# Kernel optimization log

Hardware: AMD Instinct MI355X
Metric: run time of the kernel (lower is better)

The kernel has to match this reference:

```python
import jax, jax.numpy as jnp
import numpy as np

NUM_HEADS = 12
WIN = 7  # window_size[0] == window_size[1]


def setup_inputs() -> dict:
    key = jax.random.key(0)
    ks = jax.random.split(key, 8)
    B_, N, C = 2048, WIN * WIN, 384
    nW = 64
    return {
        "x": jax.random.normal(ks[0], (B_, N, C), dtype=jnp.float32),
        "mask": jax.random.normal(ks[1], (nW, N, N), dtype=jnp.float32),
        "qkv_w": jax.random.normal(ks[2], (3 * C, C), dtype=jnp.float32) * 0.02,
        "qkv_b": jax.random.normal(ks[3], (3 * C,), dtype=jnp.float32) * 0.02,
        "proj_w": jax.random.normal(ks[4], (C, C), dtype=jnp.float32) * 0.02,
        "proj_b": jax.random.normal(ks[5], (C,), dtype=jnp.float32) * 0.02,
        "rpb_table": jax.random.normal(ks[6], ((2 * WIN - 1) ** 2, NUM_HEADS), dtype=jnp.float32) * 0.02,
        "rel_index": jax.random.randint(ks[7], (N * N,), 0, (2 * WIN - 1) ** 2, dtype=jnp.int32),
    }


def reference(x, mask, qkv_w, qkv_b, proj_w, proj_b, rpb_table, rel_index):
    B_, N, C = x.shape
    H = NUM_HEADS
    d = C // H
    scale = d ** -0.5

    # QKV projection (quant wrappers act as identity in non-quant state)
    qkv = x @ qkv_w.T + qkv_b                      # [B_, N, 3C]
    qkv = qkv.reshape(B_, N, 3, H, d).transpose(2, 0, 3, 1, 4)  # [3, B_, H, N, d]
    q, k, v = qkv[0], qkv[1], qkv[2]

    attn = jnp.einsum("bhnd,bhmd->bhnm", q * scale, k)  # [B_, H, N, N]

    # relative position bias gather: [N*N] -> [N, N, H] -> [H, N, N]
    bias = rpb_table[rel_index].reshape(N, N, H).transpose(2, 0, 1)
    attn = attn + bias[None]

    # shifted-window mask add
    nW = mask.shape[0]
    attn = attn.reshape(B_ // nW, nW, H, N, N) + mask[None, :, None]
    attn = attn.reshape(B_, H, N, N)

    attn = jax.nn.softmax(attn, axis=-1)

    out = jnp.einsum("bhnm,bhmd->bhnd", attn, v)   # [B_, H, N, d]
    out = out.transpose(0, 2, 1, 3).reshape(B_, N, C)
    out = out @ proj_w.T + proj_b
    return out, attn
```

## Files before the change

kernel.cpp:

```cpp
#include <hip/hip_runtime.h>
#include <hip/hip_bf16.h>
#include <stdint.h>

#define H_ 12
#define D_ 32
#define N_ 49
#define C_ 384
#define B_TOT 2048
#define BH 24576
#define M_ROWS 100352
#define SCALE 0.17677669529663689f

typedef float f32x4 __attribute__((ext_vector_type(4)));
typedef __bf16 bf16x8 __attribute__((ext_vector_type(8)));
typedef unsigned short ushortx8 __attribute__((ext_vector_type(8)));

static __device__ __forceinline__ unsigned short f2bf(float f) {
  __bf16 b = (__bf16)f;
  return __builtin_bit_cast(unsigned short, b);
}

static __device__ __forceinline__ uint4 pack8(float4 a, float4 b) {
  ushortx8 v;
  v[0] = f2bf(a.x); v[1] = f2bf(a.y); v[2] = f2bf(a.z); v[3] = f2bf(a.w);
  v[4] = f2bf(b.x); v[5] = f2bf(b.y); v[6] = f2bf(b.z); v[7] = f2bf(b.w);
  return __builtin_bit_cast(uint4, v);
}

#define GL16(gp, lp)                                                        \
  __builtin_amdgcn_global_load_lds(                                         \
      (const __attribute__((address_space(1))) unsigned int*)(gp),          \
      (__attribute__((address_space(3))) unsigned int*)(lp), 16, 0, 0)

__global__ void prep(const float* __restrict__ x, const float* __restrict__ wq,
                     const float* __restrict__ wpw, const float* __restrict__ mask,
                     const float* __restrict__ rpb, const int* __restrict__ ridx,
                     unsigned short* __restrict__ x_bf,
                     unsigned short* __restrict__ wq_bf,
                     unsigned short* __restrict__ wp_bf,
                     float* __restrict__ comb) {
  const int blk = blockIdx.x, tid = threadIdx.x;
  if (blk < 2048) {
    for (int i = blk * 256 + tid; i < 4816896; i += 2048 * 256) {
      float4 a = ((const float4*)x)[2 * i];
      float4 b = ((const float4*)x)[2 * i + 1];
      *(uint4*)&x_bf[(size_t)i * 8] = pack8(a, b);
    }
  } else if (blk < 2264) {
    const int i = (blk - 2048) * 256 + tid;
    float4 a = ((const float4*)wq)[2 * i];
    float4 b = ((const float4*)wq)[2 * i + 1];
    *(uint4*)&wq_bf[(size_t)i * 8] = pack8(a, b);
  } else if (blk < 2336) {
    const int i = (blk - 2264) * 256 + tid;
    float4 a = ((const float4*)wpw)[2 * i];
    float4 b = ((const float4*)wpw)[2 * i + 1];
    *(uint4*)&wp_bf[(size_t)i * 8] = pack8(a, b);
  } else {
    const int wh = blk - 2336;
    const int w = wh / 12, h = wh - w * 12;
    float* cb = comb + (size_t)wh * 4096;
    const float* mw = mask + (size_t)w * N_ * N_;
    for (int e = tid; e < 4096; e += 256) {
      const int r = e >> 6, c = e & 63;
      float v;
      if (c >= N_) v = -1e30f;
      else if (r >= N_) v = 0.0f;
      else v = mw[r * N_ + c] + rpb[ridx[r * N_ + c] * H_ + h];
      cb[(r * 16 + (c & 15)) * 4 + (c >> 4)] = v;
    }
  }
}

__global__ __launch_bounds__(256, 4)
void qkv_gemm(const unsigned short* __restrict__ A,
              const unsigned short* __restrict__ W,
              const float* __restrict__ bias, unsigned short* __restrict__ qkv) {
  __shared__ __align__(16) unsigned short smem[16384];
  const int tid = threadIdx.x;
  const int w = blockIdx.x;
  const int t = (w & 7) * 882 + (w >> 3);
  const int bm = t / 9, bn = t - bm * 9;
  const int lane = tid & 63, wv = tid >> 6;
  const int wm = wv >> 1, wn = wv & 1;
  const int lo = lane & 15, hi = lane >> 4;

  const int sr0 = tid >> 2, sq0 = (tid & 3) ^ ((sr0 >> 1) & 3);
  const int ci1 = tid + 256;
  const int sr1 = ci1 >> 2, sq1 = (ci1 & 3) ^ ((sr1 >> 1) & 3);

  const unsigned short* Ab = A + (size_t)bm * 128 * 384;
  const unsigned short* Wb = W + (size_t)bn * 128 * 384;

  f32x4 acc[4][4];
#pragma unroll
  for (int i = 0; i < 4; i++)
#pragma unroll
    for (int j = 0; j < 4; j++)
#pragma unroll
      for (int r = 0; r < 4; r++) acc[i][j][r] = 0.0f;

  {
    unsigned short* b0 = smem;
    GL16(Ab + sr0 * 384 + sq0 * 8, b0 + tid * 8);
    GL16(Ab + sr1 * 384 + sq1 * 8, b0 + ci1 * 8);
    GL16(Wb + sr0 * 384 + sq0 * 8, b0 + 4096 + tid * 8);
    GL16(Wb + sr1 * 384 + sq1 * 8, b0 + 4096 + ci1 * 8);
  }
  __syncthreads();

  int buf = 0;
  for (int kt = 0; kt < 12; kt++) {
    if (kt < 11) {
      const int kk = (kt + 1) * 32;
      unsigned short* nb = smem + (buf ^ 1) * 8192;
      GL16(Ab + sr0 * 384 + kk + sq0 * 8, nb + tid * 8);
      GL16(Ab + sr1 * 384 + kk + sq1 * 8, nb + ci1 * 8);
      GL16(Wb + sr0 * 384 + kk + sq0 * 8, nb + 4096 + tid * 8);
      GL16(Wb + sr1 * 384 + kk + sq1 * 8, nb + 4096 + ci1 * 8);
    }
    const unsigned short* ba = smem + buf * 8192;
    bf16x8 af[4], bfm[4];
#pragma unroll
    for (int mt = 0; mt < 4; mt++) {
      const int row = wm * 64 + mt * 16 + lo;
      af[mt] = *(const bf16x8*)&ba[(row * 4 + (hi ^ ((row >> 1) & 3))) * 8];
    }
#pragma unroll
    for (int nt = 0; nt < 4; nt++) {
      const int row = wn * 64 + nt * 16 + lo;
      bfm[nt] = *(const bf16x8*)&ba[4096 + (row * 4 + (hi ^ ((row >> 1) & 3))) * 8];
    }
#pragma unroll
    for (int mt = 0; mt < 4; mt++)
#pragma unroll
      for (int nt = 0; nt < 4; nt++)
        acc[mt][nt] = __builtin_amdgcn_mfma_f32_16x16x32_bf16(af[mt], bfm[nt], acc[mt][nt], 0, 0, 0);
    __syncthreads();
    buf ^= 1;
  }

  unsigned short* ep = smem + wv * 4096;
#pragma unroll
  for (int nt = 0; nt < 4; nt++) {
    const int j = bn * 128 + wn * 64 + nt * 16 + lo;
    const float bj = bias[j];
    const float mul = (j < 384) ? SCALE : 1.0f;
    const int c16 = nt * 2 + (lo >> 3);
    const int wi = lo & 7;
#pragma unroll
    for (int mt = 0; mt < 4; mt++) {
#pragma unroll
      for (int r = 0; r < 4; r++) {
        const int row = mt * 16 + hi * 4 + r;
        ep[row * 64 + ((c16 ^ hi) << 3) + wi] = f2bf((acc[mt][nt][r] + bj) * mul);
      }
    }
  }
#pragma unroll
  for (int cc = 0; cc < 2; cc++) {
    const int cidx = cc * 64 + lane;
    const int lr = cidx >> 1, lch = cidx & 1;
    const int i = bm * 128 + wm * 64 + lr;
    const int b = i / 49, sq = i - b * 49;
    const int j0 = bn * 128 + wn * 64 + lch * 32;
    const int which = j0 / 384;
    const int rem = j0 - which * 384;
    const int h = rem >> 5;
    const int hlr = (lr >> 2) & 3;
    unsigned short* dst = qkv + ((size_t)which * BH + (size_t)b * H_ + h) * (N_ * D_) + sq * D_;
#pragma unroll
    for (int q = 0; q < 4; q++) {
      const int c16r = lch * 4 + q;
      *(uint4*)(dst + q * 8) = *(const uint4*)&ep[lr * 64 + ((c16r ^ hlr) << 3)];
    }
  }
}

__global__ __launch_bounds__(64, 2)
void attn_kernel(const unsigned short* __restrict__ qkv,
                 const float* __restrict__ comb,
                 float* __restrict__ probs,
                 unsigned short* __restrict__ av) {
  __shared__ __align__(16) unsigned short P[64 * 64];
  __shared__ __align__(16) unsigned short VT[32 * 64];
  const int lane = threadIdx.x;
  const int lo = lane & 15, hi = lane >> 4;
  const int l7 = lo & 7;
  const int h = blockIdx.x, b = blockIdx.y;

  const unsigned short* qp = qkv + (size_t)(b * H_ + h) * (N_ * D_);
  const unsigned short* kp = qp + (size_t)BH * (N_ * D_);
  const unsigned short* vp = kp + (size_t)BH * (N_ * D_);

  {
    unsigned int* vz = (unsigned int*)VT;
#pragma unroll
    for (int i = 0; i < 16; i++) vz[lane + 64 * i] = 0u;
  }
  __syncthreads();

  bf16x8 aq[4], bk[4];
#pragma unroll
  for (int t = 0; t < 4; t++) {
    aq[t] = *(const bf16x8*)(qp + (t * 16 + lo) * D_ + hi * 8);
    bk[t] = *(const bf16x8*)(kp + (t * 16 + lo) * D_ + hi * 8);
  }
  f32x4 s[4][4];
#pragma unroll
  for (int mt = 0; mt < 4; mt++)
#pragma unroll
    for (int nt = 0; nt < 4; nt++) {
#pragma unroll
      for (int r = 0; r < 4; r++) s[mt][nt][r] = 0.0f;
      s[mt][nt] = __builtin_amdgcn_mfma_f32_16x16x32_bf16(aq[mt], bk[nt], s[mt][nt], 0, 0, 0);
    }

#pragma unroll
  for (int it = 0; it < 4; it++) {
    const int idx = it * 64 + lane;
    if (idx < 196) {
      const int sq = idx >> 2, ch = idx & 3;
      ushortx8 vv = *(const ushortx8*)(vp + sq * D_ + ch * 8);
#pragma unroll
      for (int jj = 0; jj < 8; jj++)
        VT[(ch * 8 + jj) * 64 + (((sq >> 3) ^ jj) << 3) + (sq & 7)] = vv[jj];
    }
  }

  const float* cb = comb + (size_t)((b & 63) * H_ + h) * 4096;
#pragma unroll
  for (int mt = 0; mt < 4; mt++) {
#pragma unroll
    for (int r = 0; r < 4; r++) {
      const int row = mt * 16 + hi * 4 + r;
      const float4 cr = *(const float4*)(cb + (row * 16 + lo) * 4);
      float v0 = s[mt][0][r] + cr.x;
      float v1 = s[mt][1][r] + cr.y;
      float v2 = s[mt][2][r] + cr.z;
      float v3 = s[mt][3][r] + cr.w;
      float m = fmaxf(fmaxf(v0, v1), fmaxf(v2, v3));
      m = fmaxf(m, __shfl_xor(m, 1));
      m = fmaxf(m, __shfl_xor(m, 2));
      m = fmaxf(m, __shfl_xor(m, 4));
      m = fmaxf(m, __shfl_xor(m, 8));
      v0 = __expf(v0 - m); v1 = __expf(v1 - m);
      v2 = __expf(v2 - m); v3 = __expf(v3 - m);
      float sum = v0 + v1 + v2 + v3;
      sum += __shfl_xor(sum, 1);
      sum += __shfl_xor(sum, 2);
      sum += __shfl_xor(sum, 4);
      sum += __shfl_xor(sum, 8);
      const float rinv = 1.0f / sum;
      s[mt][0][r] = v0 * rinv; s[mt][1][r] = v1 * rinv;
      s[mt][2][r] = v2 * rinv; s[mt][3][r] = v3 * rinv;
    }
  }

  const size_t pbase = (size_t)(b * H_ + h) * N_ * N_;
#pragma unroll
  for (int mt = 0; mt < 4; mt++) {
#pragma unroll
    for (int r = 0; r < 4; r++) {
      const int row = mt * 16 + hi * 4 + r;
      if (row < N_) {
#pragma unroll
        for (int nt = 0; nt < 4; nt++) {
          const int c = nt * 16 + lo;
          if (c < N_) probs[pbase + row * N_ + c] = s[mt][nt][r];
        }
      }
      const int r7 = row & 7;
#pragma unroll
      for (int nt = 0; nt < 4; nt++)
        P[row * 64 + (((nt * 2 + (lo >> 3)) ^ r7) << 3) + l7] = f2bf(s[mt][nt][r]);
    }
  }
  __syncthreads();

  f32x4 o[4][2];
#pragma unroll
  for (int mt = 0; mt < 4; mt++)
#pragma unroll
    for (int n2 = 0; n2 < 2; n2++)
#pragma unroll
      for (int r = 0; r < 4; r++) o[mt][n2][r] = 0.0f;
#pragma unroll
  for (int ks = 0; ks < 2; ks++) {
    bf16x8 pa[4], vb[2];
#pragma unroll
    for (int mt = 0; mt < 4; mt++)
      pa[mt] = *(const bf16x8*)&P[(mt * 16 + lo) * 64 + (((ks * 4 + hi) ^ l7) << 3)];
#pragma unroll
    for (int n2 = 0; n2 < 2; n2++)
      vb[n2] = *(const bf16x8*)&VT[(n2 * 16 + lo) * 64 + (((ks * 4 + hi) ^ l7) << 3)];
#pragma unroll
    for (int mt = 0; mt < 4; mt++)
#pragma unroll
      for (int n2 = 0; n2 < 2; n2++)
        o[mt][n2] = __builtin_amdgcn_mfma_f32_16x16x32_bf16(pa[mt], vb[n2], o[mt][n2], 0, 0, 0);
  }

  __syncthreads();
#pragma unroll
  for (int mt = 0; mt < 4; mt++) {
#pragma unroll
    for (int r = 0; r < 4; r++) {
      const int row = mt * 16 + hi * 4 + r;
      if (row < N_) {
#pragma unroll
        for (int n2 = 0; n2 < 2; n2++)
          P[row * 40 + n2 * 16 + lo] = f2bf(o[mt][n2][r]);
      }
    }
  }
  if (lane < N_) {
    unsigned short* dst = av + ((size_t)b * N_ + lane) * C_ + h * D_;
    const unsigned short* src = P + lane * 40;
#pragma unroll
    for (int q = 0; q < 4; q++)
      *(uint4*)(dst + q * 8) = *(const uint4*)(src + q * 8);
  }
}

__global__ __launch_bounds__(256, 4)
void proj_gemm(const unsigned short* __restrict__ A,
               const unsigned short* __restrict__ W,
               const float* __restrict__ bias, float* __restrict__ out) {
  __shared__ __align__(16) unsigned short smem[16384];
  const int tid = threadIdx.x;
  const int w = blockIdx.x;
  const int t = (w & 7) * 294 + (w >> 3);
  const int bm = t / 3, bn = t - bm * 3;
  const int lane = tid & 63, wv = tid >> 6;
  const int wm = wv >> 1, wn = wv & 1;
  const int lo = lane & 15, hi = lane >> 4;

  const int sr0 = tid >> 2, sq0 = (tid & 3) ^ ((sr0 >> 1) & 3);
  const int ci1 = tid + 256;
  const int sr1 = ci1 >> 2, sq1 = (ci1 & 3) ^ ((sr1 >> 1) & 3);

  const unsigned short* Ab = A + (size_t)bm * 128 * 384;
  const unsigned short* Wb = W + (size_t)bn * 128 * 384;

  f32x4 acc[4][4];
#pragma unroll
  for (int i = 0; i < 4; i++)
#pragma unroll
    for (int j = 0; j < 4; j++)
#pragma unroll
      for (int r = 0; r < 4; r++) acc[i][j][r] = 0.0f;

  {
    unsigned short* b0 = smem;
    GL16(Ab + sr0 * 384 + sq0 * 8, b0 + tid * 8);
    GL16(Ab + sr1 * 384 + sq1 * 8, b0 + ci1 * 8);
    GL16(Wb + sr0 * 384 + sq0 * 8, b0 + 4096 + tid * 8);
    GL16(Wb + sr1 * 384 + sq1 * 8, b0 + 4096 + ci1 * 8);
  }
  __syncthreads();

  int buf = 0;
  for (int kt = 0; kt < 12; kt++) {
    if (kt < 11) {
      const int kk = (kt + 1) * 32;
      unsigned short* nb = smem + (buf ^ 1) * 8192;
      GL16(Ab + sr0 * 384 + kk + sq0 * 8, nb + tid * 8);
      GL16(Ab + sr1 * 384 + kk + sq1 * 8, nb + ci1 * 8);
      GL16(Wb + sr0 * 384 + kk + sq0 * 8, nb + 4096 + tid * 8);
      GL16(Wb + sr1 * 384 + kk + sq1 * 8, nb + 4096 + ci1 * 8);
    }
    const unsigned short* ba = smem + buf * 8192;
    bf16x8 af[4], bfm[4];
#pragma unroll
    for (int mt = 0; mt < 4; mt++) {
      const int row = wm * 64 + mt * 16 + lo;
      af[mt] = *(const bf16x8*)&ba[(row * 4 + (hi ^ ((row >> 1) & 3))) * 8];
    }
#pragma unroll
    for (int nt = 0; nt < 4; nt++) {
      const int row = wn * 64 + nt * 16 + lo;
      bfm[nt] = *(const bf16x8*)&ba[4096 + (row * 4 + (hi ^ ((row >> 1) & 3))) * 8];
    }
#pragma unroll
    for (int mt = 0; mt < 4; mt++)
#pragma unroll
      for (int nt = 0; nt < 4; nt++)
        acc[mt][nt] = __builtin_amdgcn_mfma_f32_16x16x32_bf16(af[mt], bfm[nt], acc[mt][nt], 0, 0, 0);
    __syncthreads();
    buf ^= 1;
  }

#pragma unroll
  for (int nt = 0; nt < 4; nt++) {
    const int j = bn * 128 + wn * 64 + nt * 16 + lo;
    const float bj = bias[j];
#pragma unroll
    for (int mt = 0; mt < 4; mt++) {
#pragma unroll
      for (int r = 0; r < 4; r++) {
        const int i = bm * 128 + wm * 64 + mt * 16 + hi * 4 + r;
        out[(size_t)i * 384 + j] = acc[mt][nt][r] + bj;
      }
    }
  }
}

extern "C" void kernel_launch(void* const* d_in, const int* in_sizes, int n_in,
                              void* d_out, int out_size, void* d_ws, size_t ws_size,
                              hipStream_t stream) {
  const float* x      = (const float*)d_in[0];
  const float* mask   = (const float*)d_in[1];
  const float* qkv_w  = (const float*)d_in[2];
  const float* qkv_b  = (const float*)d_in[3];
  const float* proj_w = (const float*)d_in[4];
  const float* proj_b = (const float*)d_in[5];
  const float* rpb    = (const float*)d_in[6];
  const int*   ridx   = (const int*)d_in[7];

  unsigned short* qkv   = (unsigned short*)d_ws;
  unsigned short* x_bf  = qkv + (size_t)3 * BH * N_ * D_;
  unsigned short* av    = x_bf;
  float* comb           = (float*)(x_bf + (size_t)M_ROWS * C_);
  unsigned short* wq_bf = (unsigned short*)(comb + 768 * 4096);
  unsigned short* wp_bf = wq_bf + 1152 * 384;
  float* out   = (float*)d_out;
  float* probs = out + (size_t)M_ROWS * C_;

  prep<<<3104, 256, 0, stream>>>(x, qkv_w, proj_w, mask, rpb, ridx,
                                 x_bf, wq_bf, wp_bf, comb);
  qkv_gemm<<<7056, 256, 0, stream>>>(x_bf, wq_bf, qkv_b, qkv);
  attn_kernel<<<dim3(H_, B_TOT), 64, 0, stream>>>(qkv, comb, probs, av);
  proj_gemm<<<2352, 256, 0, stream>>>(av, wp_bf, proj_b, out);
}
```

Before: 458.4 us.

## Split attention kernel across four waves, one 16-row query tile each

```diff
diff --git a/kernel.cpp b/kernel.cpp
--- a/kernel.cpp
+++ b/kernel.cpp
@@ -177,14 +177,15 @@
   }
 }
 
-__global__ __launch_bounds__(64, 2)
+__global__ __launch_bounds__(256, 8)
 void attn_kernel(const unsigned short* __restrict__ qkv,
                  const float* __restrict__ comb,
                  float* __restrict__ probs,
                  unsigned short* __restrict__ av) {
   __shared__ __align__(16) unsigned short P[64 * 64];
   __shared__ __align__(16) unsigned short VT[32 * 64];
-  const int lane = threadIdx.x;
+  const int tid = threadIdx.x;
+  const int wv = tid >> 6, lane = tid & 63;
   const int lo = lane & 15, hi = lane >> 4;
   const int l7 = lo & 7;
   const int h = blockIdx.x, b = blockIdx.y;
@@ -196,127 +197,100 @@
   {
     unsigned int* vz = (unsigned int*)VT;
 #pragma unroll
-    for (int i = 0; i < 16; i++) vz[lane + 64 * i] = 0u;
-  }
-  __syncthreads();
-
-  bf16x8 aq[4], bk[4];
-#pragma unroll
-  for (int t = 0; t < 4; t++) {
-    aq[t] = *(const bf16x8*)(qp + (t * 16 + lo) * D_ + hi * 8);
+    for (int i = 0; i < 8; i++) vz[tid + 256 * i] = 0u;
+  }
+  __syncthreads();
+
+  bf16x8 aq = *(const bf16x8*)(qp + (wv * 16 + lo) * D_ + hi * 8);
+  bf16x8 bk[4];
+#pragma unroll
+  for (int t = 0; t < 4; t++)
     bk[t] = *(const bf16x8*)(kp + (t * 16 + lo) * D_ + hi * 8);
-  }
-  f32x4 s[4][4];
-#pragma unroll
-  for (int mt = 0; mt < 4; mt++)
-#pragma unroll
-    for (int nt = 0; nt < 4; nt++) {
-#pragma unroll
-      for (int r = 0; r < 4; r++) s[mt][nt][r] = 0.0f;
-      s[mt][nt] = __builtin_amdgcn_mfma_f32_16x16x32_bf16(aq[mt], bk[nt], s[mt][nt], 0, 0, 0);
-    }
-
-#pragma unroll
-  for (int it = 0; it < 4; it++) {
-    const int idx = it * 64 + lane;
-    if (idx < 196) {
-      const int sq = idx >> 2, ch = idx & 3;
-      ushortx8 vv = *(const ushortx8*)(vp + sq * D_ + ch * 8);
-#pragma unroll
-      for (int jj = 0; jj < 8; jj++)
-        VT[(ch * 8 + jj) * 64 + (((sq >> 3) ^ jj) << 3) + (sq & 7)] = vv[jj];
-    }
+
+  f32x4 s[4];
+#pragma unroll
+  for (int nt = 0; nt < 4; nt++) {
+#pragma unroll
+    for (int r = 0; r < 4; r++) s[nt][r] = 0.0f;
+    s[nt] = __builtin_amdgcn_mfma_f32_16x16x32_bf16(aq, bk[nt], s[nt], 0, 0, 0);
+  }
+
+  if (tid < 196) {
+    const int sq = tid >> 2, ch = tid & 3;
+    ushortx8 vv = *(const ushortx8*)(vp + sq * D_ + ch * 8);
+#pragma unroll
+    for (int jj = 0; jj < 8; jj++)
+      VT[(ch * 8 + jj) * 64 + (((sq >> 3) ^ jj) << 3) + (sq & 7)] = vv[jj];
   }
 
   const float* cb = comb + (size_t)((b & 63) * H_ + h) * 4096;
-#pragma unroll
-  for (int mt = 0; mt < 4; mt++) {
-#pragma unroll
-    for (int r = 0; r < 4; r++) {
-      const int row = mt * 16 + hi * 4 + r;
-      const float4 cr = *(const float4*)(cb + (row * 16 + lo) * 4);
-      float v0 = s[mt][0][r] + cr.x;
-      float v1 = s[mt][1][r] + cr.y;
-      float v2 = s[mt][2][r] + cr.z;
-      float v3 = s[mt][3][r] + cr.w;
-      float m = fmaxf(fmaxf(v0, v1), fmaxf(v2, v3));
-      m = fmaxf(m, __shfl_xor(m, 1));
-      m = fmaxf(m, __shfl_xor(m, 2));
-      m = fmaxf(m, __shfl_xor(m, 4));
-      m = fmaxf(m, __shfl_xor(m, 8));
-      v0 = __expf(v0 - m); v1 = __expf(v1 - m);
-      v2 = __expf(v2 - m); v3 = __expf(v3 - m);
-      float sum = v0 + v1 + v2 + v3;
-      sum += __shfl_xor(sum, 1);
-      sum += __shfl_xor(sum, 2);
-      sum += __shfl_xor(sum, 4);
-      sum += __shfl_xor(sum, 8);
-      const float rinv = 1.0f / sum;
-      s[mt][0][r] = v0 * rinv; s[mt][1][r] = v1 * rinv;
-      s[mt][2][r] = v2 * rinv; s[mt][3][r] = v3 * rinv;
-    }
-  }
-
   const size_t pbase = (size_t)(b * H_ + h) * N_ * N_;
 #pragma unroll
-  for (int mt = 0; mt < 4; mt++) {
-#pragma unroll
-    for (int r = 0; r < 4; r++) {
-      const int row = mt * 16 + hi * 4 + r;
-      if (row < N_) {
-#pragma unroll
-        for (int nt = 0; nt < 4; nt++) {
-          const int c = nt * 16 + lo;
-          if (c < N_) probs[pbase + row * N_ + c] = s[mt][nt][r];
-        }
-      }
-      const int r7 = row & 7;
-#pragma unroll
-      for (int nt = 0; nt < 4; nt++)
-        P[row * 64 + (((nt * 2 + (lo >> 3)) ^ r7) << 3) + l7] = f2bf(s[mt][nt][r]);
-    }
-  }
-  __syncthreads();
-
-  f32x4 o[4][2];
-#pragma unroll
-  for (int mt = 0; mt < 4; mt++)
-#pragma unroll
-    for (int n2 = 0; n2 < 2; n2++)
-#pragma unroll
-      for (int r = 0; r < 4; r++) o[mt][n2][r] = 0.0f;
+  for (int r = 0; r < 4; r++) {
+    const int row = wv * 16 + hi * 4 + r;
+    const float4 cr = *(const float4*)(cb + (row * 16 + lo) * 4);
+    float v0 = s[0][r] + cr.x;
+    float v1 = s[1][r] + cr.y;
+    float v2 = s[2][r] + cr.z;
+    float v3 = s[3][r] + cr.w;
+    float m = fmaxf(fmaxf(v0, v1), fmaxf(v2, v3));
+    m = fmaxf(m, __shfl_xor(m, 1));
+    m = fmaxf(m, __shfl_xor(m, 2));
+    m = fmaxf(m, __shfl_xor(m, 4));
+    m = fmaxf(m, __shfl_xor(m, 8));
+    v0 = __expf(v0 - m); v1 = __expf(v1 - m);
+    v2 = __expf(v2 - m); v3 = __expf(v3 - m);
+    float sum = v0 + v1 + v2 + v3;
+    sum += __shfl_xor(sum, 1);
+    sum += __shfl_xor(sum, 2);
+    sum += __shfl_xor(sum, 4);
+    sum += __shfl_xor(sum, 8);
+    const float rinv = 1.0f / sum;
+    v0 *= rinv; v1 *= rinv; v2 *= rinv; v3 *= rinv;
+
+    if (row < N_) {
+      probs[pbase + row * N_ + lo] = v0;
+      probs[pbase + row * N_ + 16 + lo] = v1;
+      probs[pbase + row * N_ + 32 + lo] = v2;
+      if (lo < 1) probs[pbase + row * N_ + 48 + lo] = v3;
+    }
+    const int r7 = row & 7;
+    P[row * 64 + ((((lo >> 3)) ^ r7) << 3) + l7] = f2bf(v0);
+    P[row * 64 + (((2 + (lo >> 3)) ^ r7) << 3) + l7] = f2bf(v1);
+    P[row * 64 + (((4 + (lo >> 3)) ^ r7) << 3) + l7] = f2bf(v2);
+    P[row * 64 + (((6 + (lo >> 3)) ^ r7) << 3) + l7] = f2bf(v3);
+  }
+  __syncthreads();
+
+  f32x4 o[2];
+#pragma unroll
+  for (int n2 = 0; n2 < 2; n2++)
+#pragma unroll
+    for (int r = 0; r < 4; r++) o[n2][r] = 0.0f;
 #pragma unroll
   for (int ks = 0; ks < 2; ks++) {
-    bf16x8 pa[4], vb[2];
-#pragma unroll
-    for (int mt = 0; mt < 4; mt++)
-      pa[mt] = *(const bf16x8*)&P[(mt * 16 + lo) * 64 + (((ks * 4 + hi) ^ l7) << 3)];
-#pragma unroll
-    for (int n2 = 0; n2 < 2; n2++)
-      vb[n2] = *(const bf16x8*)&VT[(n2 * 16 + lo) * 64 + (((ks * 4 + hi) ^ l7) << 3)];
-#pragma unroll
-    for (int mt = 0; mt < 4; mt++)
-#pragma unroll
-      for (int n2 = 0; n2 < 2; n2++)
-        o[mt][n2] = __builtin_amdgcn_mfma_f32_16x16x32_bf16(pa[mt], vb[n2], o[mt][n2], 0, 0, 0);
-  }
-
-  __syncthreads();
-#pragma unroll
-  for (int mt = 0; mt < 4; mt++) {
-#pragma unroll
-    for (int r = 0; r < 4; r++) {
-      const int row = mt * 16 + hi * 4 + r;
-      if (row < N_) {
-#pragma unroll
-        for (int n2 = 0; n2 < 2; n2++)
-          P[row * 40 + n2 * 16 + lo] = f2bf(o[mt][n2][r]);
-      }
-    }
-  }
-  if (lane < N_) {
-    unsigned short* dst = av + ((size_t)b * N_ + lane) * C_ + h * D_;
-    const unsigned short* src = P + lane * 40;
+    bf16x8 pa = *(const bf16x8*)&P[(wv * 16 + lo) * 64 + (((ks * 4 + hi) ^ l7) << 3)];
+    bf16x8 vb0 = *(const bf16x8*)&VT[lo * 64 + (((ks * 4 + hi) ^ l7) << 3)];
+    bf16x8 vb1 = *(const bf16x8*)&VT[(16 + lo) * 64 + (((ks * 4 + hi) ^ l7) << 3)];
+    o[0] = __builtin_amdgcn_mfma_f32_16x16x32_bf16(pa, vb0, o[0], 0, 0, 0);
+    o[1] = __builtin_amdgcn_mfma_f32_16x16x32_bf16(pa, vb1, o[1], 0, 0, 0);
+  }
+
+  __syncthreads();
+
+#pragma unroll
+  for (int r = 0; r < 4; r++) {
+    const int row = wv * 16 + hi * 4 + r;
+    if (row < N_) {
+      P[row * 40 + lo] = f2bf(o[0][r]);
+      P[row * 40 + 16 + lo] = f2bf(o[1][r]);
+    }
+  }
+  __syncthreads();
+
+  if (tid < N_) {
+    unsigned short* dst = av + ((size_t)b * N_ + tid) * C_ + h * D_;
+    const unsigned short* src = P + tid * 40;
 #pragma unroll
     for (int q = 0; q < 4; q++)
       *(uint4*)(dst + q * 8) = *(const uint4*)(src + q * 8);
@@ -430,6 +404,6 @@
   prep<<<3104, 256, 0, stream>>>(x, qkv_w, proj_w, mask, rpb, ridx,
                                  x_bf, wq_bf, wp_bf, comb);
   qkv_gemm<<<7056, 256, 0, stream>>>(x_bf, wq_bf, qkv_b, qkv);
-  attn_kernel<<<dim3(H_, B_TOT), 64, 0, stream>>>(qkv, comb, probs, av);
+  attn_kernel<<<dim3(H_, B_TOT), 256, 0, stream>>>(qkv, comb, probs, av);
   proj_gemm<<<2352, 256, 0, stream>>>(av, wp_bf, proj_b, out);
 }
```

Measured after the change: 473.6 us. +3.3%, slower.
